# Optimization experiments

Hardware: AMD Instinct MI355X
Metric: run time of the kernel (lower is better)

## Reference

```python
import math
import jax, jax.numpy as jnp
import numpy as np


def _alibi_slopes(n_heads: int) -> np.ndarray:
    def pow2_slopes(n):
        start = 2 ** (-2 ** (-(math.log2(n) - 3)))
        return [start * (start ** i) for i in range(n)]
    if n_heads & (n_heads - 1) == 0:
        slopes = pow2_slopes(n_heads)
    else:
        closest = 2 ** math.floor(math.log2(n_heads))
        slopes = pow2_slopes(closest)
        extra_base = 2 ** (-2 ** (-(math.log2(2 * closest) - 3)))
        slopes.extend(extra_base * (extra_base ** i) for i in range(n_heads - closest))
        slopes = slopes[:n_heads]
    return np.asarray(slopes, dtype=np.float32)


def setup_inputs() -> dict:
    B, T, C, H = 2, 2048, 768, 12
    key = jax.random.key(0)
    ks = jax.random.split(key, 6)
    return {
        "x_norm_for_qk": jax.random.normal(ks[0], (B, T, C), jnp.float32),
        "xt_current_for_v": jax.random.normal(ks[1], (B, T, C), jnp.float32),
        "W_attn": jax.random.normal(ks[2], (2 * C, C), jnp.float32) * 0.02,  # nn.Linear weight [out,in]
        "b_attn": jnp.zeros((2 * C,), jnp.float32),
        "v_tmp": jax.random.normal(ks[3], (H, H), jnp.float32) * 0.02,
        "proj_tmp": jax.random.normal(ks[4], (H, H), jnp.float32) * 0.02,
    }


def reference(x_norm_for_qk, xt_current_for_v, W_attn, b_attn, v_tmp, proj_tmp):
    B, T, C = x_norm_for_qk.shape
    H = v_tmp.shape[0]
    hd = C // H

    # Q,K projection: Linear(C -> 2C), then split.
    qk = x_norm_for_qk @ W_attn.T + b_attn  # [B,T,2C]
    q, k = jnp.split(qk, 2, axis=-1)
    q = q.reshape(B, T, H, hd).transpose(0, 2, 1, 3)  # [B,H,T,hd]
    k = k.reshape(B, T, H, hd).transpose(0, 2, 1, 3)

    # Kronecker-lifted V: block (i,j) of the CxC matrix is v_tmp[i,j]*I(hd),
    # so applying it mixes only across heads per head-dim channel.
    xt = xt_current_for_v.reshape(B, T, H, hd)
    v = jnp.einsum("ij,btjd->btid", v_tmp, xt).transpose(0, 2, 1, 3)  # [B,H,T,hd]

    scale = 1.0 / math.sqrt(hd)
    scores = jnp.einsum("bhqd,bhkd->bhqk", q, k) * scale  # [B,H,T,T]

    # ALiBi bias with causal mask (-inf above diagonal).
    slopes = jnp.asarray(_alibi_slopes(H))  # [H]
    pos = jnp.arange(T, dtype=jnp.float32)
    rel = pos[None, :] - pos[:, None]  # [T,T], memory - context
    causal = pos[None, :] <= pos[:, None]
    bias = jnp.where(causal[None], slopes[:, None, None] * rel[None], -jnp.inf)  # [H,T,T]
    scores = scores + bias[None]

    att = jax.nn.softmax(scores, axis=-1)  # dropout p=0 -> identity
    y = jnp.einsum("bhqk,bhkd->bhqd", att, v)  # [B,H,T,hd]
    y = y.transpose(0, 2, 1, 3)  # [B,T,H,hd]

    # Kronecker-lifted output projection.
    y = jnp.einsum("ij,btjd->btid", proj_tmp, y)
    return y.reshape(B, T, C)
```

## Files before the change

### kernel.cpp

```cpp
#include <hip/hip_runtime.h>
#include <hip/hip_bf16.h>
#include <math.h>

#define TSEQ 2048
#define CDIM 768
#define NH   12
#define HD   64

typedef __attribute__((ext_vector_type(8))) short bf16x8;
typedef __attribute__((ext_vector_type(4))) float f32x4;

union Bf8 { bf16x8 v; __hip_bfloat16 e[8]; };

__constant__ float c_slopes2[12] = {
    0.72134752f, 0.36067376f, 0.18033688f, 0.09016844f,
    0.04508422f, 0.02254211f, 0.011271055f, 0.0056355275f,
    1.02015692f, 0.72134752f, 0.51007846f, 0.36067376f
};
#define M2 4.3280851f
#define QSCALE 0.18033688f
#define EXP2F(x) __builtin_amdgcn_exp2f(x)

__device__ __forceinline__ unsigned pack2(float lo, float hi) {
    union { __hip_bfloat162 b; unsigned u; } cv;
    cv.b = __float22bfloat162_rn(make_float2(lo, hi));
    return cv.u;
}
__device__ __forceinline__ unsigned short bf16bits(float x) {
    union { __hip_bfloat16 b; unsigned short s; } cv;
    cv.b = __float2bfloat16(x);
    return cv.s;
}
__device__ __forceinline__ void gload16(const __hip_bfloat16* g, char* l) {
    __builtin_amdgcn_global_load_lds(
        (const __attribute__((address_space(1))) void*)g,
        (__attribute__((address_space(3))) void*)l, 16, 0, 0);
}

#define MFMA16(a, b, c) __builtin_amdgcn_mfma_f32_16x16x32_bf16(a, b, c, 0, 0, 0)
#define WAITV8 asm volatile("s_waitcnt vmcnt(8)" ::: "memory");
#define WAITV0 asm volatile("s_waitcnt vmcnt(0)" ::: "memory");

__global__ __launch_bounds__(256) void gemm_qk(
    const float* __restrict__ X,
    const float* __restrict__ W,
    const float* __restrict__ bias,
    __hip_bfloat16* __restrict__ Qb,
    __hip_bfloat16* __restrict__ Kb)
{
    __shared__ alignas(16) __hip_bfloat16 As[128][40];
    __shared__ alignas(16) __hip_bfloat16 Bs[128][40];

    const int tid  = threadIdx.x;
    const int lane = tid & 63;
    const int w    = tid >> 6;
    const int lg   = lane >> 4;
    const int lc   = lane & 15;
    const int m0   = blockIdx.y * 128;
    const int n0   = blockIdx.x * 128;
    const int m0w  = (w >> 1) * 64;
    const int n0w  = (w & 1) * 64;

    const int srow = tid >> 3;
    const int scol = (tid & 7) * 4;

    f32x4 acc[4][4] = {};

    for (int k0 = 0; k0 < CDIM; k0 += 32) {
        __syncthreads();
        #pragma unroll
        for (int r = 0; r < 4; ++r) {
            int row = r * 32 + srow;
            float4 a = *(const float4*)(X + (size_t)(m0 + row) * CDIM + k0 + scol);
            float4 b = *(const float4*)(W + (size_t)(n0 + row) * CDIM + k0 + scol);
            As[row][scol+0] = __float2bfloat16(a.x);
            As[row][scol+1] = __float2bfloat16(a.y);
            As[row][scol+2] = __float2bfloat16(a.z);
            As[row][scol+3] = __float2bfloat16(a.w);
            Bs[row][scol+0] = __float2bfloat16(b.x);
            Bs[row][scol+1] = __float2bfloat16(b.y);
            Bs[row][scol+2] = __float2bfloat16(b.z);
            Bs[row][scol+3] = __float2bfloat16(b.w);
        }
        __syncthreads();

        bf16x8 af[4], bfr[4];
        #pragma unroll
        for (int mt = 0; mt < 4; ++mt)
            af[mt] = *(const bf16x8*)&As[m0w + mt*16 + lc][lg*8];
        #pragma unroll
        for (int nt = 0; nt < 4; ++nt)
            bfr[nt] = *(const bf16x8*)&Bs[n0w + nt*16 + lc][lg*8];
        #pragma unroll
        for (int mt = 0; mt < 4; ++mt)
            #pragma unroll
            for (int nt = 0; nt < 4; ++nt)
                acc[mt][nt] = MFMA16(af[mt], bfr[nt], acc[mt][nt]);
    }

    #pragma unroll
    for (int mt = 0; mt < 4; ++mt) {
        #pragma unroll
        for (int nt = 0; nt < 4; ++nt) {
            int n  = n0 + n0w + nt*16 + lc;
            float bv = bias[n];
            #pragma unroll
            for (int r = 0; r < 4; ++r) {
                int m = m0 + m0w + mt*16 + lg*4 + r;
                float v = acc[mt][nt][r] + bv;
                int b = m >> 11, t = m & (TSEQ-1);
                if (n < CDIM) {
                    int h = n >> 6, dd = n & 63;
                    Qb[(((size_t)(b*NH + h))*TSEQ + t)*HD + dd] = __float2bfloat16(v * QSCALE);
                } else {
                    int n2 = n - CDIM;
                    int h = n2 >> 6, dd = n2 & 63;
                    Kb[(((size_t)(b*NH + h))*TSEQ + t)*HD + dd] = __float2bfloat16(v);
                }
            }
        }
    }
}

__global__ __launch_bounds__(256) void vmix(
    const float* __restrict__ XT, const float* __restrict__ vtmp,
    __hip_bfloat16* __restrict__ Vb)
{
    __shared__ float vm[144];
    if (threadIdx.x < 144) vm[threadIdx.x] = vtmp[threadIdx.x];
    __syncthreads();
    int idx = blockIdx.x * 256 + threadIdx.x;
    int dd = idx & 63;
    int bt = idx >> 6;
    int t = bt & (TSEQ-1), b = bt >> 11;
    float xv[12];
    #pragma unroll
    for (int j = 0; j < 12; ++j) xv[j] = XT[(size_t)bt*CDIM + j*64 + dd];
    #pragma unroll
    for (int i = 0; i < 12; ++i) {
        float s = 0.f;
        #pragma unroll
        for (int j = 0; j < 12; ++j) s += vm[i*12+j] * xv[j];
        Vb[(((size_t)(b*NH + i))*TSEQ + t)*HD + dd] = __float2bfloat16(s);
    }
}

__global__ __launch_bounds__(256) void vtrans(
    const __hip_bfloat16* __restrict__ Vb, __hip_bfloat16* __restrict__ Vt)
{
    __shared__ __hip_bfloat16 Ls[64][65];
    const int bh = blockIdx.y;
    const int t0 = blockIdx.x * 64;
    const int tid = threadIdx.x;
    const int r8 = tid >> 3;
    const int c8 = (tid & 7) * 8;

    #pragma unroll
    for (int it = 0; it < 2; ++it) {
        int t = it*32 + r8;
        Bf8 v; v.v = *(const bf16x8*)(Vb + ((size_t)bh*TSEQ + t0 + t)*HD + c8);
        #pragma unroll
        for (int j = 0; j < 8; ++j) Ls[t][c8 + j] = v.e[j];
    }
    __syncthreads();
    #pragma unroll
    for (int it = 0; it < 2; ++it) {
        int d = it*32 + r8;
        Bf8 v;
        #pragma unroll
        for (int j = 0; j < 8; ++j) v.e[j] = Ls[c8 + j][d];
        *(bf16x8*)(Vt + ((size_t)bh*HD + d)*TSEQ + t0 + c8) = v.v;
    }
}

__global__ __launch_bounds__(128) void attn6(
    const __hip_bfloat16* __restrict__ Qb,
    const __hip_bfloat16* __restrict__ Kb,
    const __hip_bfloat16* __restrict__ Vt,
    __hip_bfloat16* __restrict__ Y)
{
    __shared__ alignas(16) char stage[2][2][8192];
    __shared__ alignas(16) float comb[2][16][68];
    __shared__ float lcomb[2][16];

    const int tid  = threadIdx.x;
    const int lane = tid & 63;
    const int w    = tid >> 6;
    const int lg   = lane >> 4;
    const int lc   = lane & 15;

    const int id  = blockIdx.x;
    const int id2 = (id & 7) * 96 + (id >> 3);
    const int bx  = id2 & 31;
    const int bh  = id2 >> 5;

    const float slope = c_slopes2[bh % NH];
    const __hip_bfloat16* Qp = Qb + (size_t)bh * TSEQ * HD;
    const __hip_bfloat16* Kp = Kb + (size_t)bh * TSEQ * HD;
    const __hip_bfloat16* Vp = Vt + (size_t)bh * HD * TSEQ;

    const int kRow = lane >> 3;
    const int kCh  = ((lane & 7) ^ kRow) * 8;
    const int vRow = lane >> 2;
    const int vCh  = ((lane & 3) ^ ((lane >> 3) & 3)) * 8;

    char* myStage = &stage[w][0][0];
    const float slgl   = slope * (float)(lg * 4);
    const float slp16  = slope * 16.0f;
    const int   s01    = lc + ((lg & 1) << 5);
    const int   s23    = s01 + 16;
    const bool  hiK    = (lg >= 2);

#define ISSUE(K0, BUF) do {                                                     \
    char* db_ = myStage + (BUF)*8192;                                           \
    const __hip_bfloat16* kg_ = Kp + (size_t)((K0) + kRow)*HD + kCh;            \
    gload16(kg_,           db_);                                                \
    gload16(kg_ +  8*HD,   db_ + 1024);                                         \
    gload16(kg_ + 16*HD,   db_ + 2048);                                         \
    gload16(kg_ + 24*HD,   db_ + 3072);                                         \
    const __hip_bfloat16* vg_ = Vp + (size_t)vRow*TSEQ + (K0) + vCh;            \
    gload16(vg_,           db_ + 4096);                                         \
    gload16(vg_ + 16*TSEQ, db_ + 5120);                                         \
    gload16(vg_ + 32*TSEQ, db_ + 6144);                                         \
    gload16(vg_ + 48*TSEQ, db_ + 7168);                                         \
} while (0);

#define SHUF(P_, x0, x1, x2, x3)                                                \
    {                                                                           \
        int t00 = __shfl((int)x0, s01), t02 = __shfl((int)x2, s01);             \
        int t10 = __shfl((int)x1, s01), t12 = __shfl((int)x3, s01);             \
        int t20 = __shfl((int)x0, s23), t22 = __shfl((int)x2, s23);             \
        int t30 = __shfl((int)x1, s23), t32 = __shfl((int)x3, s23);             \
        P_.u[0] = hiK ? (unsigned)t02 : (unsigned)t00;                          \
        P_.u[1] = hiK ? (unsigned)t12 : (unsigned)t10;                          \
        P_.u[2] = hiK ? (unsigned)t22 : (unsigned)t20;                          \
        P_.u[3] = hiK ? (unsigned)t32 : (unsigned)t30;                          \
    }

#define CONS(K0C, BUF, MASKED) do {                                             \
    const char* bK_ = myStage + (BUF)*8192;                                     \
    const char* bV_ = bK_ + 4096;                                               \
    const int swzk_ = lc & 7;                                                   \
    const char* kr0_ = bK_ + lc*128;                                            \
    const char* kr1_ = bK_ + (16 + lc)*128;                                     \
    bf16x8 k0lo = *(const bf16x8*)(kr0_ + (((lg    ) ^ swzk_) << 4));           \
    bf16x8 k0hi = *(const bf16x8*)(kr0_ + (((lg + 4) ^ swzk_) << 4));           \
    bf16x8 k1lo = *(const bf16x8*)(kr1_ + (((lg    ) ^ swzk_) << 4));           \
    bf16x8 k1hi = *(const bf16x8*)(kr1_ + (((lg + 4) ^ swzk_) << 4));           \
    f32x4 s0a = {}, s0b = {}, s1a = {}, s1b = {};                               \
    s0a = MFMA16(k0lo, qfa0, s0a); s0a = MFMA16(k0hi, qfa1, s0a);               \
    s0b = MFMA16(k0lo, qfb0, s0b); s0b = MFMA16(k0hi, qfb1, s0b);               \
    s1a = MFMA16(k1lo, qfa0, s1a); s1a = MFMA16(k1hi, qfa1, s1a);               \
    s1b = MFMA16(k1lo, qfb0, s1b); s1b = MFMA16(k1hi, qfb1, s1b);               \
    float base0_ = fmaf((float)(K0C), slope, slgl);                             \
    float pa0[4], pa1[4], pb0[4], pb1[4];                                       \
    _Pragma("unroll")                                                           \
    for (int r = 0; r < 4; ++r) {                                               \
        float bk_  = base0_ + slope * (float)r;                                 \
        float bk1_ = bk_ + slp16;                                               \
        pa0[r] = EXP2F(s0a[r] + (bk_  - eqa));                                  \
        pa1[r] = EXP2F(s1a[r] + (bk1_ - eqa));                                  \
        pb0[r] = EXP2F(s0b[r] + (bk_  - eqb));                                  \
        pb1[r] = EXP2F(s1b[r] + (bk1_ - eqb));                                  \
        if (MASKED) {                                                           \
            int kk0_ = (K0C) + lg*4 + r, kk1_ = kk0_ + 16;                      \
            if (kk0_ > qia) pa0[r] = 0.f;                                       \
            if (kk1_ > qia) pa1[r] = 0.f;                                       \
            if (kk0_ > qib) pb0[r] = 0.f;                                       \
            if (kk1_ > qib) pb1[r] = 0.f;                                       \
        }                                                                       \
        lsa += pa0[r] + pa1[r];                                                 \
        lsb += pb0[r] + pb1[r];                                                 \
    }                                                                           \
    unsigned a0_ = pack2(pa0[0], pa0[1]), a1_ = pack2(pa0[2], pa0[3]);          \
    unsigned a2_ = pack2(pa1[0], pa1[1]), a3_ = pack2(pa1[2], pa1[3]);          \
    unsigned b0_ = pack2(pb0[0], pb0[1]), b1_ = pack2(pb0[2], pb0[3]);          \
    unsigned b2_ = pack2(pb1[0], pb1[1]), b3_ = pack2(pb1[2], pb1[3]);          \
    union { unsigned u[4]; bf16x8 v; } PA_, PB_;                                \
    SHUF(PA_, a0_, a1_, a2_, a3_)                                               \
    SHUF(PB_, b0_, b1_, b2_, b3_)                                               \
    const int swzv_ = (lc >> 1) & 3;                                            \
    _Pragma("unroll")                                                           \
    for (int dt = 0; dt < 4; ++dt) {                                            \
        bf16x8 vf_ = *(const bf16x8*)(bV_ + (dt*16 + lc)*64 + ((lg ^ swzv_) << 4)); \
        Oa[dt] = MFMA16(vf_, PA_.v, Oa[dt]);                                    \
        Ob[dt] = MFMA16(vf_, PB_.v, Ob[dt]);                                    \
    }                                                                           \
} while (0);

    auto runMember = [&](int qb, bool first) {
        const int q0m = qb * 32;
        const int qia = q0m + lc;
        const int qib = q0m + 16 + lc;
        const float eqa = slope * (float)qia + M2;
        const float eqb = slope * (float)qib + M2;

        bf16x8 qfa0 = *(const bf16x8*)(Qp + (size_t)qia * HD + lg*8);
        bf16x8 qfa1 = *(const bf16x8*)(Qp + (size_t)qia * HD + 32 + lg*8);
        bf16x8 qfb0 = *(const bf16x8*)(Qp + (size_t)qib * HD + lg*8);
        bf16x8 qfb1 = *(const bf16x8*)(Qp + (size_t)qib * HD + 32 + lg*8);

        f32x4 Oa[4] = {}; f32x4 Ob[4] = {};
        float lsa = 0.f, lsb = 0.f;

        const int  myN     = (qb >= w) ? ((qb - w) >> 1) + 1 : 0;
        const bool ownDiag = (myN > 0) && ((qb & 1) == w);
        const int  nFull   = myN - (ownDiag ? 1 : 0);

        if (myN > 0) {
            ISSUE(w * 32, 0)
            int j = 0;
            for (; j < nFull; ++j) {
                const int k0c = (w + 2*j) * 32;
                if (j + 1 < myN) { ISSUE((w + 2*(j+1)) * 32, (j+1) & 1) WAITV8 }
                else             { WAITV0 }
                CONS(k0c, j & 1, false)
            }
            if (ownDiag) {
                WAITV0
                CONS((w + 2*j) * 32, j & 1, true)
            }
        }

        lsa += __shfl_xor(lsa, 16); lsa += __shfl_xor(lsa, 32);
        lsb += __shfl_xor(lsb, 16); lsb += __shfl_xor(lsb, 32);

        if (!first) __syncthreads();
        if (w == 0) {
            #pragma unroll
            for (int dt = 0; dt < 4; ++dt)
                *(f32x4*)&comb[0][lc][dt*16 + lg*4] = Ob[dt];
            if (lane < 16) lcomb[0][lane] = lsb;
        } else {
            #pragma unroll
            for (int dt = 0; dt < 4; ++dt)
                *(f32x4*)&comb[1][lc][dt*16 + lg*4] = Oa[dt];
            if (lane < 16) lcomb[1][lane] = lsa;
        }
        __syncthreads();

        const int q = q0m + w*16 + lc;
        float lt  = ((w == 0) ? lsa : lsb) + lcomb[1 ^ w][lc];
        float inv = 1.0f / lt;
        #pragma unroll
        for (int dt = 0; dt < 4; ++dt) {
            f32x4 o = (w == 0) ? Oa[dt] : Ob[dt];
            o += *(const f32x4*)&comb[1 ^ w][lc][dt*16 + lg*4];
            ushort4 u;
            u.x = bf16bits(o[0] * inv);
            u.y = bf16bits(o[1] * inv);
            u.z = bf16bits(o[2] * inv);
            u.w = bf16bits(o[3] * inv);
            *(ushort4*)(Y + ((size_t)bh*TSEQ + q)*HD + dt*16 + lg*4) = u;
        }
    };

    runMember(bx, true);
    runMember(63 - bx, false);

#undef ISSUE
#undef SHUF
#undef CONS
}

__global__ __launch_bounds__(256) void projmix(
    const __hip_bfloat16* __restrict__ Y, const float* __restrict__ ptmp,
    float* __restrict__ Out)
{
    __shared__ float pm[144];
    if (threadIdx.x < 144) pm[threadIdx.x] = ptmp[threadIdx.x];
    __syncthreads();
    int idx = blockIdx.x * 256 + threadIdx.x;
    int dd = idx & 63;
    int bt = idx >> 6;
    int t = bt & (TSEQ-1), b = bt >> 11;
    float yv[12];
    #pragma unroll
    for (int j = 0; j < 12; ++j)
        yv[j] = __bfloat162float(Y[(((size_t)(b*NH + j))*TSEQ + t)*HD + dd]);
    #pragma unroll
    for (int i = 0; i < 12; ++i) {
        float s = 0.f;
        #pragma unroll
        for (int j = 0; j < 12; ++j) s += pm[i*12+j] * yv[j];
        Out[(size_t)bt*CDIM + i*64 + dd] = s;
    }
}

extern "C" void kernel_launch(void* const* d_in, const int* in_sizes, int n_in,
                              void* d_out, int out_size, void* d_ws, size_t ws_size,
                              hipStream_t stream) {
    (void)in_sizes; (void)n_in; (void)out_size; (void)ws_size;
    const float* X    = (const float*)d_in[0];
    const float* XT   = (const float*)d_in[1];
    const float* W    = (const float*)d_in[2];
    const float* bias = (const float*)d_in[3];
    const float* vtmp = (const float*)d_in[4];
    const float* ptmp = (const float*)d_in[5];
    float* Out = (float*)d_out;

    char* ws = (char*)d_ws;
    const size_t BHTD = (size_t)2 * NH * TSEQ * HD;
    __hip_bfloat16* Qb = (__hip_bfloat16*)ws;
    __hip_bfloat16* Kb = (__hip_bfloat16*)(ws + BHTD*2);
    __hip_bfloat16* Vb = (__hip_bfloat16*)(ws + BHTD*4);
    __hip_bfloat16* Vt = (__hip_bfloat16*)(ws + BHTD*6);
    __hip_bfloat16* Yb = (__hip_bfloat16*)(ws + BHTD*8);

    gemm_qk<<<dim3(12, 32), 256, 0, stream>>>(X, W, bias, Qb, Kb);
    vmix<<<1024, 256, 0, stream>>>(XT, vtmp, Vb);
    vtrans<<<dim3(32, 24), 256, 0, stream>>>(Vb, Vt);
    attn6<<<768, 128, 0, stream>>>(Qb, Kb, Vt, Yb);
    projmix<<<1024, 256, 0, stream>>>(Yb, ptmp, Out);
}
```

Before: 94.41 us.

## Load V fragments directly to registers in MFMA-ready tiled layout; widen QK GEMM block

The V-transpose kernel now writes V in a 32-key tiled layout so each attention lane can load its MFMA operand fragments straight from global memory into registers. This removes the V staging through LDS. The attention loop double-buffers those register fragments, and the separate masked diagonal pass becomes an always-applied select. The QK projection GEMM moves to 512 threads with a 64x32 tile per wave and vectorized 16-byte LDS stores. The trade-off is more register pressure under launch_bounds(128,4) and masking work on every tile.

```diff
diff --git a/kernel.cpp b/kernel.cpp
--- a/kernel.cpp
+++ b/kernel.cpp
@@ -41,7 +41,7 @@
 #define WAITV8 asm volatile("s_waitcnt vmcnt(8)" ::: "memory");
 #define WAITV0 asm volatile("s_waitcnt vmcnt(0)" ::: "memory");
 
-__global__ __launch_bounds__(256) void gemm_qk(
+__global__ __launch_bounds__(512) void gemm_qk(
     const float* __restrict__ X,
     const float* __restrict__ W,
     const float* __restrict__ bias,
@@ -58,50 +58,55 @@
     const int lc   = lane & 15;
     const int m0   = blockIdx.y * 128;
     const int n0   = blockIdx.x * 128;
-    const int m0w  = (w >> 1) * 64;
-    const int n0w  = (w & 1) * 64;
-
-    const int srow = tid >> 3;
-    const int scol = (tid & 7) * 4;
-
-    f32x4 acc[4][4] = {};
+    const int m0w  = (w >> 2) * 64;
+    const int n0w  = (w & 3) * 32;
+
+    const int srow = tid >> 2;
+    const int scol = (tid & 3) * 8;
+
+    f32x4 acc[4][2] = {};
 
     for (int k0 = 0; k0 < CDIM; k0 += 32) {
         __syncthreads();
-        #pragma unroll
-        for (int r = 0; r < 4; ++r) {
-            int row = r * 32 + srow;
-            float4 a = *(const float4*)(X + (size_t)(m0 + row) * CDIM + k0 + scol);
-            float4 b = *(const float4*)(W + (size_t)(n0 + row) * CDIM + k0 + scol);
-            As[row][scol+0] = __float2bfloat16(a.x);
-            As[row][scol+1] = __float2bfloat16(a.y);
-            As[row][scol+2] = __float2bfloat16(a.z);
-            As[row][scol+3] = __float2bfloat16(a.w);
-            Bs[row][scol+0] = __float2bfloat16(b.x);
-            Bs[row][scol+1] = __float2bfloat16(b.y);
-            Bs[row][scol+2] = __float2bfloat16(b.z);
-            Bs[row][scol+3] = __float2bfloat16(b.w);
+        {
+            const float* xp = X + (size_t)(m0 + srow) * CDIM + k0 + scol;
+            const float* wp = W + (size_t)(n0 + srow) * CDIM + k0 + scol;
+            float4 a0 = *(const float4*)(xp);
+            float4 a1 = *(const float4*)(xp + 4);
+            float4 b0 = *(const float4*)(wp);
+            float4 b1 = *(const float4*)(wp + 4);
+            Bf8 av, bv;
+            av.e[0]=__float2bfloat16(a0.x); av.e[1]=__float2bfloat16(a0.y);
+            av.e[2]=__float2bfloat16(a0.z); av.e[3]=__float2bfloat16(a0.w);
+            av.e[4]=__float2bfloat16(a1.x); av.e[5]=__float2bfloat16(a1.y);
+            av.e[6]=__float2bfloat16(a1.z); av.e[7]=__float2bfloat16(a1.w);
+            bv.e[0]=__float2bfloat16(b0.x); bv.e[1]=__float2bfloat16(b0.y);
+            bv.e[2]=__float2bfloat16(b0.z); bv.e[3]=__float2bfloat16(b0.w);
+            bv.e[4]=__float2bfloat16(b1.x); bv.e[5]=__float2bfloat16(b1.y);
+            bv.e[6]=__float2bfloat16(b1.z); bv.e[7]=__float2bfloat16(b1.w);
+            *(bf16x8*)&As[srow][scol] = av.v;
+            *(bf16x8*)&Bs[srow][scol] = bv.v;
         }
         __syncthreads();
 
-        bf16x8 af[4], bfr[4];
+        bf16x8 af[4], bfr[2];
         #pragma unroll
         for (int mt = 0; mt < 4; ++mt)
             af[mt] = *(const bf16x8*)&As[m0w + mt*16 + lc][lg*8];
         #pragma unroll
-        for (int nt = 0; nt < 4; ++nt)
+        for (int nt = 0; nt < 2; ++nt)
             bfr[nt] = *(const bf16x8*)&Bs[n0w + nt*16 + lc][lg*8];
         #pragma unroll
         for (int mt = 0; mt < 4; ++mt)
             #pragma unroll
-            for (int nt = 0; nt < 4; ++nt)
+            for (int nt = 0; nt < 2; ++nt)
                 acc[mt][nt] = MFMA16(af[mt], bfr[nt], acc[mt][nt]);
     }
 
     #pragma unroll
     for (int mt = 0; mt < 4; ++mt) {
         #pragma unroll
-        for (int nt = 0; nt < 4; ++nt) {
+        for (int nt = 0; nt < 2; ++nt) {
             int n  = n0 + n0w + nt*16 + lc;
             float bv = bias[n];
             #pragma unroll
@@ -169,17 +174,19 @@
         Bf8 v;
         #pragma unroll
         for (int j = 0; j < 8; ++j) v.e[j] = Ls[c8 + j][d];
-        *(bf16x8*)(Vt + ((size_t)bh*HD + d)*TSEQ + t0 + c8) = v.v;
-    }
-}
-
-__global__ __launch_bounds__(128) void attn6(
+        int kb = (t0 + c8) >> 5;
+        int ko = (t0 + c8) & 31;
+        *(bf16x8*)(Vt + (size_t)bh*(HD*TSEQ) + kb*2048 + d*32 + ko) = v.v;
+    }
+}
+
+__global__ __launch_bounds__(128, 4) void attn7(
     const __hip_bfloat16* __restrict__ Qb,
     const __hip_bfloat16* __restrict__ Kb,
     const __hip_bfloat16* __restrict__ Vt,
     __hip_bfloat16* __restrict__ Y)
 {
-    __shared__ alignas(16) char stage[2][2][8192];
+    __shared__ alignas(16) char kstage[2][2][4096];
     __shared__ alignas(16) float comb[2][16][68];
     __shared__ float lcomb[2][16];
 
@@ -197,32 +204,33 @@
     const float slope = c_slopes2[bh % NH];
     const __hip_bfloat16* Qp = Qb + (size_t)bh * TSEQ * HD;
     const __hip_bfloat16* Kp = Kb + (size_t)bh * TSEQ * HD;
-    const __hip_bfloat16* Vp = Vt + (size_t)bh * HD * TSEQ;
+    const __hip_bfloat16* Vp = Vt + (size_t)bh * (HD * TSEQ);
 
     const int kRow = lane >> 3;
     const int kCh  = ((lane & 7) ^ kRow) * 8;
-    const int vRow = lane >> 2;
-    const int vCh  = ((lane & 3) ^ ((lane >> 3) & 3)) * 8;
-
-    char* myStage = &stage[w][0][0];
-    const float slgl   = slope * (float)(lg * 4);
-    const float slp16  = slope * 16.0f;
-    const int   s01    = lc + ((lg & 1) << 5);
-    const int   s23    = s01 + 16;
-    const bool  hiK    = (lg >= 2);
-
-#define ISSUE(K0, BUF) do {                                                     \
-    char* db_ = myStage + (BUF)*8192;                                           \
+
+    char* myK = &kstage[w][0][0];
+    const float slgl  = slope * (float)(lg * 4);
+    const float slp16 = slope * 16.0f;
+    const int   s01   = lc + ((lg & 1) << 5);
+    const int   s23   = s01 + 16;
+    const bool  hiK   = (lg >= 2);
+
+#define ISSK(K0, BUF) do {                                                      \
+    char* db_ = myK + (BUF)*4096;                                               \
     const __hip_bfloat16* kg_ = Kp + (size_t)((K0) + kRow)*HD + kCh;            \
-    gload16(kg_,           db_);                                                \
-    gload16(kg_ +  8*HD,   db_ + 1024);                                         \
-    gload16(kg_ + 16*HD,   db_ + 2048);                                         \
-    gload16(kg_ + 24*HD,   db_ + 3072);                                         \
-    const __hip_bfloat16* vg_ = Vp + (size_t)vRow*TSEQ + (K0) + vCh;            \
-    gload16(vg_,           db_ + 4096);                                         \
-    gload16(vg_ + 16*TSEQ, db_ + 5120);                                         \
-    gload16(vg_ + 32*TSEQ, db_ + 6144);                                         \
-    gload16(vg_ + 48*TSEQ, db_ + 7168);                                         \
+    gload16(kg_,         db_);                                                  \
+    gload16(kg_ +  8*HD, db_ + 1024);                                           \
+    gload16(kg_ + 16*HD, db_ + 2048);                                           \
+    gload16(kg_ + 24*HD, db_ + 3072);                                           \
+} while (0);
+
+#define VLOADX(P0, P1, P2, P3, K0) do {                                         \
+    const __hip_bfloat16* vb_ = Vp + (size_t)((K0) >> 5) * 2048 + lc*32 + lg*8; \
+    P0 = *(const bf16x8*)(vb_);                                                 \
+    P1 = *(const bf16x8*)(vb_ + 512);                                           \
+    P2 = *(const bf16x8*)(vb_ + 1024);                                          \
+    P3 = *(const bf16x8*)(vb_ + 1536);                                          \
 } while (0);
 
 #define SHUF(P_, x0, x1, x2, x3)                                                \
@@ -237,9 +245,8 @@
         P_.u[3] = hiK ? (unsigned)t32 : (unsigned)t30;                          \
     }
 
-#define CONS(K0C, BUF, MASKED) do {                                             \
-    const char* bK_ = myStage + (BUF)*8192;                                     \
-    const char* bV_ = bK_ + 4096;                                               \
+#define CONS(K0C, BUF, V0_, V1_, V2_, V3_) do {                                 \
+    const char* bK_ = myK + (BUF)*4096;                                         \
     const int swzk_ = lc & 7;                                                   \
     const char* kr0_ = bK_ + lc*128;                                            \
     const char* kr1_ = bK_ + (16 + lc)*128;                                     \
@@ -258,17 +265,15 @@
     for (int r = 0; r < 4; ++r) {                                               \
         float bk_  = base0_ + slope * (float)r;                                 \
         float bk1_ = bk_ + slp16;                                               \
-        pa0[r] = EXP2F(s0a[r] + (bk_  - eqa));                                  \
-        pa1[r] = EXP2F(s1a[r] + (bk1_ - eqa));                                  \
-        pb0[r] = EXP2F(s0b[r] + (bk_  - eqb));                                  \
-        pb1[r] = EXP2F(s1b[r] + (bk1_ - eqb));                                  \
-        if (MASKED) {                                                           \
-            int kk0_ = (K0C) + lg*4 + r, kk1_ = kk0_ + 16;                      \
-            if (kk0_ > qia) pa0[r] = 0.f;                                       \
-            if (kk1_ > qia) pa1[r] = 0.f;                                       \
-            if (kk0_ > qib) pb0[r] = 0.f;                                       \
-            if (kk1_ > qib) pb1[r] = 0.f;                                       \
-        }                                                                       \
+        int kk0_ = (K0C) + lg*4 + r, kk1_ = kk0_ + 16;                          \
+        float e0a = EXP2F(s0a[r] + (bk_  - eqa));                               \
+        float e1a = EXP2F(s1a[r] + (bk1_ - eqa));                               \
+        float e0b = EXP2F(s0b[r] + (bk_  - eqb));                               \
+        float e1b = EXP2F(s1b[r] + (bk1_ - eqb));                               \
+        pa0[r] = (kk0_ <= qia) ? e0a : 0.f;                                     \
+        pa1[r] = (kk1_ <= qia) ? e1a : 0.f;                                     \
+        pb0[r] = (kk0_ <= qib) ? e0b : 0.f;                                     \
+        pb1[r] = (kk1_ <= qib) ? e1b : 0.f;                                     \
         lsa += pa0[r] + pa1[r];                                                 \
         lsb += pb0[r] + pb1[r];                                                 \
     }                                                                           \
@@ -279,13 +284,10 @@
     union { unsigned u[4]; bf16x8 v; } PA_, PB_;                                \
     SHUF(PA_, a0_, a1_, a2_, a3_)                                               \
     SHUF(PB_, b0_, b1_, b2_, b3_)                                               \
-    const int swzv_ = (lc >> 1) & 3;                                            \
-    _Pragma("unroll")                                                           \
-    for (int dt = 0; dt < 4; ++dt) {                                            \
-        bf16x8 vf_ = *(const bf16x8*)(bV_ + (dt*16 + lc)*64 + ((lg ^ swzv_) << 4)); \
-        Oa[dt] = MFMA16(vf_, PA_.v, Oa[dt]);                                    \
-        Ob[dt] = MFMA16(vf_, PB_.v, Ob[dt]);                                    \
-    }                                                                           \
+    Oa[0] = MFMA16(V0_, PA_.v, Oa[0]); Ob[0] = MFMA16(V0_, PB_.v, Ob[0]);       \
+    Oa[1] = MFMA16(V1_, PA_.v, Oa[1]); Ob[1] = MFMA16(V1_, PB_.v, Ob[1]);       \
+    Oa[2] = MFMA16(V2_, PA_.v, Oa[2]); Ob[2] = MFMA16(V2_, PB_.v, Ob[2]);       \
+    Oa[3] = MFMA16(V3_, PA_.v, Oa[3]); Ob[3] = MFMA16(V3_, PB_.v, Ob[3]);       \
 } while (0);
 
     auto runMember = [&](int qb, bool first) {
@@ -303,22 +305,31 @@
         f32x4 Oa[4] = {}; f32x4 Ob[4] = {};
         float lsa = 0.f, lsb = 0.f;
 
-        const int  myN     = (qb >= w) ? ((qb - w) >> 1) + 1 : 0;
-        const bool ownDiag = (myN > 0) && ((qb & 1) == w);
-        const int  nFull   = myN - (ownDiag ? 1 : 0);
+        const int myN = (qb >= w) ? ((qb - w) >> 1) + 1 : 0;
+
+        bf16x8 vA0, vA1, vA2, vA3, vB0, vB1, vB2, vB3;
 
         if (myN > 0) {
-            ISSUE(w * 32, 0)
+            ISSK(w*32, 0)
+            VLOADX(vA0, vA1, vA2, vA3, w*32)
             int j = 0;
-            for (; j < nFull; ++j) {
-                const int k0c = (w + 2*j) * 32;
-                if (j + 1 < myN) { ISSUE((w + 2*(j+1)) * 32, (j+1) & 1) WAITV8 }
-                else             { WAITV0 }
-                CONS(k0c, j & 1, false)
-            }
-            if (ownDiag) {
-                WAITV0
-                CONS((w + 2*j) * 32, j & 1, true)
+            while (true) {
+                if (j + 1 < myN) {
+                    const int kn = (w + 2*(j+1)) * 32;
+                    ISSK(kn, (j+1) & 1)
+                    VLOADX(vB0, vB1, vB2, vB3, kn)
+                    WAITV8
+                } else { WAITV0 }
+                CONS((w + 2*j)*32, j & 1, vA0, vA1, vA2, vA3)
+                ++j; if (j >= myN) break;
+                if (j + 1 < myN) {
+                    const int kn = (w + 2*(j+1)) * 32;
+                    ISSK(kn, (j+1) & 1)
+                    VLOADX(vA0, vA1, vA2, vA3, kn)
+                    WAITV8
+                } else { WAITV0 }
+                CONS((w + 2*j)*32, j & 1, vB0, vB1, vB2, vB3)
+                ++j; if (j >= myN) break;
             }
         }
 
@@ -358,7 +369,8 @@
     runMember(bx, true);
     runMember(63 - bx, false);
 
-#undef ISSUE
+#undef ISSK
+#undef VLOADX
 #undef SHUF
 #undef CONS
 }
@@ -407,9 +419,9 @@
     __hip_bfloat16* Vt = (__hip_bfloat16*)(ws + BHTD*6);
     __hip_bfloat16* Yb = (__hip_bfloat16*)(ws + BHTD*8);
 
-    gemm_qk<<<dim3(12, 32), 256, 0, stream>>>(X, W, bias, Qb, Kb);
+    gemm_qk<<<dim3(12, 32), 512, 0, stream>>>(X, W, bias, Qb, Kb);
     vmix<<<1024, 256, 0, stream>>>(XT, vtmp, Vb);
     vtrans<<<dim3(32, 24), 256, 0, stream>>>(Vb, Vt);
-    attn6<<<768, 128, 0, stream>>>(Qb, Kb, Vt, Yb);
+    attn7<<<768, 128, 0, stream>>>(Qb, Kb, Vt, Yb);
     projmix<<<1024, 256, 0, stream>>>(Yb, ptmp, Out);
 }
```

After: 93.32 us. No clear change (-1.2%).
